# Performance work log

Hardware: AMD Instinct MI355X
Metric: run time of the kernel (lower is better)

Reference implementation:

```python
import jax, jax.numpy as jnp
import numpy as np

B, T, E = 1024, 256, 300  # batch, topic_size, embedding_size


def setup_inputs() -> dict:
    key = jax.random.key(0)
    k1, k2, k3, k4, k5 = jax.random.split(key, 5)
    return {
        "req_theta": jax.random.uniform(k1, (B, T), dtype=jnp.float32),
        "wsdl_theta": jax.random.uniform(k2, (B, T), dtype=jnp.float32),
        "topic_embedding": jax.random.normal(k3, (E, T), dtype=jnp.float32),
        "w_f": jax.random.normal(k4, (T, E), dtype=jnp.float32) * 0.05,
        "b_f": jax.random.normal(k5, (T,), dtype=jnp.float32) * 0.05,
    }


def reference(req_theta, wsdl_theta, topic_embedding, w_f, b_f):
    # topic_embedding: [E, T] -> t(): [T, E]
    t_te = topic_embedding.T  # [T, E]
    # elementwise scale of topic vectors by theta: [B, T, E]
    req_e = req_theta[:, :, None] * t_te
    wsdl_e = wsdl_theta[:, :, None] * t_te
    # f_att: Linear(E, T): [B, T, E] -> [B, T, T]
    req_e = jnp.einsum('bte,fe->btf', req_e, w_f) + b_f
    wsdl_e = jnp.einsum('bte,fe->btf', wsdl_e, w_f) + b_f
    # cross-attention: bmm -> softmax(dim=1) -> permute -> bmm
    att = jnp.einsum('bik,bjk->bij', req_e, wsdl_e)          # [B, T, T]
    att = jax.nn.softmax(att, axis=1)                         # softmax over req dim
    wsdl_att = jnp.einsum('bji,bjk->bik', att, req_e)         # att^T @ req_e
    # mean-pool + cosine similarity * 3
    ave_req = req_e.mean(axis=1)    # [B, T]
    ave_wsdl = wsdl_att.mean(axis=1)  # [B, T]
    eps = 1e-8
    num = jnp.sum(ave_req * ave_wsdl, axis=-1)
    denom = jnp.maximum(jnp.linalg.norm(ave_req, axis=-1) * jnp.linalg.norm(ave_wsdl, axis=-1), eps)
    bi_dist = (num / denom) * 3.0
    return bi_dist
```

## Files before the change

kernel.cpp:

```cpp
#include <hip/hip_runtime.h>
#include <math.h>

constexpr int NB = 1024;
constexpr int NT = 256;
constexpr int NE = 300;

typedef float f32x2 __attribute__((ext_vector_type(2)));
typedef float f32x4 __attribute__((ext_vector_type(4)));

#if defined(__has_builtin)
#if __has_builtin(__builtin_amdgcn_exp2f)
#define EXP2F(x) __builtin_amdgcn_exp2f(x)
#else
#define EXP2F(x) exp2f(x)
#endif
#if __has_builtin(__builtin_amdgcn_logf)
#define LOG2F(x) __builtin_amdgcn_logf(x)
#else
#define LOG2F(x) log2f(x)
#endif
#else
#define EXP2F(x) exp2f(x)
#define LOG2F(x) log2f(x)
#endif

__device__ __forceinline__ float rdlane(float v, int l) {
  return __uint_as_float(__builtin_amdgcn_readlane(__float_as_uint(v), l));
}

__device__ __forceinline__ f32x2 pk_fma_alo(f32x2 a, f32x2 b, f32x2 c) {
  f32x2 d;
  asm("v_pk_fma_f32 %0, %1, %2, %3 op_sel:[0,0,0] op_sel_hi:[0,1,1]"
      : "=v"(d) : "v"(a), "v"(b), "v"(c));
  return d;
}
__device__ __forceinline__ f32x2 pk_fma_ahi(f32x2 a, f32x2 b, f32x2 c) {
  f32x2 d;
  asm("v_pk_fma_f32 %0, %1, %2, %3 op_sel:[1,0,0] op_sel_hi:[1,1,1]"
      : "=v"(d) : "v"(a), "v"(b), "v"(c));
  return d;
}
__device__ __forceinline__ f32x2 pk_fma_chi(f32x2 a, f32x2 b, f32x2 c) {
  f32x2 d;
  asm("v_pk_fma_f32 %0, %1, %2, %3 op_sel:[0,0,1] op_sel_hi:[1,1,1]"
      : "=v"(d) : "v"(a), "v"(b), "v"(c));
  return d;
}

__global__ __launch_bounds__(1024) void k_M(const float* __restrict__ TE,
                                            const float* __restrict__ wf,
                                            float* __restrict__ Mt,
                                            float* __restrict__ Mrow) {
  __shared__ float red[4][NT];
  int tid = threadIdx.x;
  int q = __builtin_amdgcn_readfirstlane(tid >> 8);
  int c = tid & 255, lane = tid & 63, blk = blockIdx.x;

  const float* wrow = wf + blk * NE;
  float4 wa = *(const float4*)(wrow + 4 * lane);
  float4 wb = make_float4(0.f, 0.f, 0.f, 0.f);
  if (lane < 11) wb = *(const float4*)(wrow + 256 + 4 * lane);
  float acc = 0.f;
#pragma unroll
  for (int k = 0; k < 16; ++k) {
    int ec = q + 4 * k;
    float wx = rdlane(wa.x, ec), wy = rdlane(wa.y, ec);
    float wz = rdlane(wa.z, ec), ww = rdlane(wa.w, ec);
    const float* tp = TE + 4 * ec * NT + c;
    acc = fmaf(tp[0], wx, acc);
    acc = fmaf(tp[NT], wy, acc);
    acc = fmaf(tp[2 * NT], wz, acc);
    acc = fmaf(tp[3 * NT], ww, acc);
  }
#pragma unroll
  for (int k = 16; k < 19; ++k) {
    int ec = q + 4 * k;
    if (ec < 75) {
      int l = ec - 64;
      float wx = rdlane(wb.x, l), wy = rdlane(wb.y, l);
      float wz = rdlane(wb.z, l), ww = rdlane(wb.w, l);
      const float* tp = TE + 4 * ec * NT + c;
      acc = fmaf(tp[0], wx, acc);
      acc = fmaf(tp[NT], wy, acc);
      acc = fmaf(tp[2 * NT], wz, acc);
      acc = fmaf(tp[3 * NT], ww, acc);
    }
  }
  red[q][c] = acc;
  __syncthreads();
  if (q == 0) {
    float s = red[0][c] + red[1][c] + red[2][c] + red[3][c];
    Mt[blk * NT + c] = s;
    Mrow[c * NT + blk] = s;
  }
}

__global__ __launch_bounds__(1024) void k_G(const float* __restrict__ Mt,
                                            const float* __restrict__ Mrow,
                                            const float* __restrict__ bf,
                                            float* __restrict__ G2,
                                            float* __restrict__ u2,
                                            float* __restrict__ Gd,
                                            float* __restrict__ Gof) {
  __shared__ float red[4][NT];
  __shared__ float fin2[4][2];
  const float LOG2E = 1.4426950408889634f;
  int tid = threadIdx.x;
  int q = __builtin_amdgcn_readfirstlane(tid >> 8);
  int c = tid & 255, lane = tid & 63, wid = tid >> 6, blk = blockIdx.x;

  const float* mrowp = Mrow + blk * NT;
  float4 ma = *(const float4*)(mrowp + 4 * lane);
  float acc = 0.f;
  int c0 = q * 16;
#pragma unroll
  for (int k = 0; k < 16; ++k) {
    int fc = c0 + k;
    float mx = rdlane(ma.x, fc), my = rdlane(ma.y, fc);
    float mz = rdlane(ma.z, fc), mw = rdlane(ma.w, fc);
    const float* tp = Mt + 4 * fc * NT + c;
    acc = fmaf(tp[0], mx, acc);
    acc = fmaf(tp[NT], my, acc);
    acc = fmaf(tp[2 * NT], mz, acc);
    acc = fmaf(tp[3 * NT], mw, acc);
  }
  red[q][c] = acc;
  __syncthreads();
  if (q == 0) {
    float g = (red[0][c] + red[1][c] + red[2][c] + red[3][c]) * LOG2E;
    G2[blk * NT + c] = g;
    if (c == blk) Gd[blk] = g;
    float v = (c == blk) ? -3.0e38f : g;
#pragma unroll
    for (int off = 32; off > 0; off >>= 1) v = fmaxf(v, __shfl_down(v, off, 64));
    if (lane == 0) fin2[wid][0] = v;
    float p = mrowp[c] * bf[c];
#pragma unroll
    for (int off = 32; off > 0; off >>= 1) p += __shfl_down(p, off, 64);
    if (lane == 0) fin2[wid][1] = p;
  }
  __syncthreads();
  if (tid == 0) {
    float gof = fmaxf(fmaxf(fin2[0][0], fin2[1][0]), fmaxf(fin2[2][0], fin2[3][0]));
    Gof[blk] = fmaxf(gof, 0.f);
    u2[blk] = (fin2[0][1] + fin2[1][1] + fin2[2][1] + fin2[3][1]) * LOG2E;
  }
}

__global__ __launch_bounds__(512, 8) void k_main(
    const float* __restrict__ req, const float* __restrict__ wsdl,
    const float* __restrict__ Mrow, const float* __restrict__ G2,
    const float* __restrict__ u2, const float* __restrict__ Gd,
    const float* __restrict__ Gof, const float* __restrict__ bf,
    float* __restrict__ out) {
  __shared__ f32x2 sArr[NT];
  __shared__ f32x2 WL[NT];
  __shared__ f32x2 QB[NT];
  __shared__ f32x4 MHN4[64];
  __shared__ f32x4 RRB[2][8][64];
  __shared__ float finU[4];
  __shared__ float fin[4][3];

  int tid = threadIdx.x;
  int cq = tid & 63, q = tid >> 6;
  int c4 = cq * 4;
  int b = blockIdx.x, i0 = q * 32;

  if (tid < NT) {
    float r = req[b * NT + tid];
    float u = u2[tid];
    sArr[tid] = (f32x2){r, u};
    WL[tid] = (f32x2){wsdl[b * NT + tid], 0.f};
    float um = fmaxf(u, 0.f);
#pragma unroll
    for (int off = 32; off > 0; off >>= 1) um = fmaxf(um, __shfl_down(um, off, 64));
    if ((tid & 63) == 0) finU[tid >> 6] = um;
  }

  f32x4 rcP = *(const f32x4*)(req + b * NT + c4);
  f32x4 wbP = *(const f32x4*)(wsdl + b * NT + c4);
  f32x4 ucP = *(const f32x4*)(u2 + c4);
  f32x4 gdP = *(const f32x4*)(Gd + c4);
  f32x4 gofP = *(const f32x4*)(Gof + c4);

  __syncthreads();
  float up = fmaxf(fmaxf(finU[0], finU[1]), fmaxf(finU[2], finU[3]));

  f32x4 mhn;
  mhn.x = -fmaxf(rcP.x * fmaf(wbP.x, gdP.x, ucP.x), fmaf(wbP.x, gofP.x, up));
  mhn.y = -fmaxf(rcP.y * fmaf(wbP.y, gdP.y, ucP.y), fmaf(wbP.y, gofP.y, up));
  mhn.z = -fmaxf(rcP.z * fmaf(wbP.z, gdP.z, ucP.z), fmaf(wbP.z, gofP.z, up));
  mhn.w = -fmaxf(rcP.w * fmaf(wbP.w, gdP.w, ucP.w), fmaf(wbP.w, gofP.w, up));
  if (q == 0) MHN4[cq] = mhn;

  f32x2 wb01 = (f32x2){wbP.x, wbP.y}, wb23 = (f32x2){wbP.z, wbP.w};
  f32x2 rc01 = (f32x2){rcP.x, rcP.y}, rc23 = (f32x2){rcP.z, rcP.w};
  f32x2 uc01 = (f32x2){ucP.x, ucP.y}, uc23 = (f32x2){ucP.z, ucP.w};
  f32x2 mhn01 = (f32x2){mhn.x, mhn.y}, mhn23 = (f32x2){mhn.z, mhn.w};

  float d0 = 0.f, d1 = 0.f, d2 = 0.f, d3 = 0.f;
  {
    const float* gp = G2 + i0 * NT + c4;
    const char* sb = (const char*)(sArr + i0);
#pragma unroll 2
    for (int o = 0; o < 8; ++o) {
#pragma unroll
      for (int uu = 0; uu < 4; ++uu) {
        f32x4 gP = *(const f32x4*)(gp + uu * NT);
        f32x2 su = *(const f32x2*)(sb + uu * 8);
        f32x2 g01 = (f32x2){gP.x, gP.y}, g23 = (f32x2){gP.z, gP.w};
        f32x2 t01 = pk_fma_chi(wb01, g01, su);
        f32x2 t23 = pk_fma_chi(wb23, g23, su);
        f32x2 p01 = pk_fma_alo(su, t01, mhn01);
        f32x2 p23 = pk_fma_alo(su, t23, mhn23);
        d0 += EXP2F(p01.x); d1 += EXP2F(p01.y);
        d2 += EXP2F(p23.x); d3 += EXP2F(p23.y);
      }
      gp += 4 * NT;
      sb += 32;
    }
  }
  RRB[0][q][cq] = (f32x4){d0, d1, d2, d3};
  __syncthreads();

  if (tid < NT) {
    const float* rb = (const float*)RRB;
    float den = rb[tid];
#pragma unroll
    for (int k = 1; k < 8; ++k) den += rb[k * 256 + tid];
    float nl = ((const float*)MHN4)[tid] - LOG2F(den);
    ((float*)(WL + tid))[1] = nl;
  }
  __syncthreads();

  float S0 = 0.f, S1 = 0.f, S2 = 0.f, S3 = 0.f;
  {
    const float* gp = G2 + i0 * NT + c4;
    const char* wb_ = (const char*)(WL + i0);
#pragma unroll 2
    for (int o = 0; o < 8; ++o) {
#pragma unroll
      for (int uu = 0; uu < 4; ++uu) {
        f32x4 gP = *(const f32x4*)(gp + uu * NT);
        f32x2 wl = *(const f32x2*)(wb_ + uu * 8);
        f32x2 g01 = (f32x2){gP.x, gP.y}, g23 = (f32x2){gP.z, gP.w};
        f32x2 t01 = pk_fma_alo(wl, g01, uc01);
        f32x2 t23 = pk_fma_alo(wl, g23, uc23);
        f32x2 p01 = pk_fma_chi(rc01, t01, wl);
        f32x2 p23 = pk_fma_chi(rc23, t23, wl);
        S0 += EXP2F(p01.x); S1 += EXP2F(p01.y);
        S2 += EXP2F(p23.x); S3 += EXP2F(p23.y);
      }
      gp += 4 * NT;
      wb_ += 32;
    }
  }
  RRB[0][q][cq] = (f32x4){S0, S1, S2, S3};
  __syncthreads();

  if (tid < NT) {
    const float* rb = (const float*)RRB;
    float Sr = rb[tid];
#pragma unroll
    for (int k = 1; k < 8; ++k) Sr += rb[k * 256 + tid];
    f32x2 ru = sArr[tid];
    QB[tid] = (f32x2){ru.x, ru.x * Sr};
  }
  __syncthreads();

  f32x2 a01 = (f32x2){0.f, 0.f}, a23 = a01, y01 = a01, y23 = a01;
  {
    const float* mp = Mrow + i0 * NT + c4;
    const char* qb_ = (const char*)(QB + i0);
#pragma unroll 2
    for (int o = 0; o < 8; ++o) {
#pragma unroll
      for (int uu = 0; uu < 4; ++uu) {
        f32x4 mkP = *(const f32x4*)(mp + uu * NT);
        f32x2 qb = *(const f32x2*)(qb_ + uu * 8);
        f32x2 mk01 = (f32x2){mkP.x, mkP.y}, mk23 = (f32x2){mkP.z, mkP.w};
        a01 = pk_fma_alo(qb, mk01, a01);
        a23 = pk_fma_alo(qb, mk23, a23);
        y01 = pk_fma_ahi(qb, mk01, y01);
        y23 = pk_fma_ahi(qb, mk23, y23);
      }
      mp += 4 * NT;
      qb_ += 32;
    }
  }
  RRB[0][q][cq] = (f32x4){a01.x, a01.y, a23.x, a23.y};
  RRB[1][q][cq] = (f32x4){y01.x, y01.y, y23.x, y23.y};
  __syncthreads();

  if (tid < NT) {
    const float* rb = (const float*)RRB;
    float A = rb[tid], Y = rb[2048 + tid];
#pragma unroll
    for (int k = 1; k < 8; ++k) {
      A += rb[k * 256 + tid];
      Y += rb[2048 + k * 256 + tid];
    }
    float bfc = bf[tid];
    const float invT = 1.0f / NT;
    float avr = fmaf(A, invT, bfc);
    float avw = fmaf(Y, invT, bfc);
    float sn = avr * avw, sa = avr * avr, sc = avw * avw;
#pragma unroll
    for (int off = 32; off > 0; off >>= 1) {
      sn += __shfl_down(sn, off, 64);
      sa += __shfl_down(sa, off, 64);
      sc += __shfl_down(sc, off, 64);
    }
    if ((tid & 63) == 0) {
      int w = tid >> 6;
      fin[w][0] = sn;
      fin[w][1] = sa;
      fin[w][2] = sc;
    }
  }
  __syncthreads();
  if (tid == 0) {
    float N = fin[0][0] + fin[1][0] + fin[2][0] + fin[3][0];
    float A = fin[0][1] + fin[1][1] + fin[2][1] + fin[3][1];
    float C = fin[0][2] + fin[1][2] + fin[2][2] + fin[3][2];
    out[b] = N / fmaxf(sqrtf(A) * sqrtf(C), 1e-8f) * 3.0f;
  }
}

extern "C" void kernel_launch(void* const* d_in, const int* in_sizes, int n_in,
                              void* d_out, int out_size, void* d_ws, size_t ws_size,
                              hipStream_t stream) {
  const float* req  = (const float*)d_in[0];
  const float* wsdl = (const float*)d_in[1];
  const float* TE   = (const float*)d_in[2];
  const float* wf   = (const float*)d_in[3];
  const float* bf   = (const float*)d_in[4];
  float* out = (float*)d_out;

  float* Mt   = (float*)d_ws;
  float* Mrow = Mt + NT * NT;
  float* G2   = Mrow + NT * NT;
  float* u2   = G2 + NT * NT;
  float* Gd   = u2 + NT;
  float* Gof  = Gd + NT;

  k_M<<<NT, 1024, 0, stream>>>(TE, wf, Mt, Mrow);
  k_G<<<NT, 1024, 0, stream>>>(Mt, Mrow, bf, G2, u2, Gd, Gof);
  k_main<<<NB, 512, 0, stream>>>(req, wsdl, Mrow, G2, u2, Gd, Gof, bf, out);
}
```

Baseline: 102.7 us.

## Process two batch rows per block to reuse G2 and Mrow loads

Each k_main block now handles two batch elements, so every G2 and Mrow tile loaded from global memory feeds computation for both rows. Shared-memory buffers widen to f32x4 to hold per-batch values, and the grid shrinks to 512 blocks. This halves global/L2 traffic for the shared matrices, at the cost of higher register use (launch bounds relaxed from 8 to 4) and fewer blocks to fill the GPU.

```diff
diff --git a/kernel.cpp b/kernel.cpp
--- a/kernel.cpp
+++ b/kernel.cpp
@@ -4,6 +4,7 @@
 constexpr int NB = 1024;
 constexpr int NT = 256;
 constexpr int NE = 300;
+constexpr int NBATCH = 2;
 
 typedef float f32x2 __attribute__((ext_vector_type(2)));
 typedef float f32x4 __attribute__((ext_vector_type(4)));
@@ -28,6 +29,11 @@
   return __uint_as_float(__builtin_amdgcn_readlane(__float_as_uint(v), l));
 }
 
+__device__ __forceinline__ f32x2 pk_fma(f32x2 a, f32x2 b, f32x2 c) {
+  f32x2 d;
+  asm("v_pk_fma_f32 %0, %1, %2, %3" : "=v"(d) : "v"(a), "v"(b), "v"(c));
+  return d;
+}
 __device__ __forceinline__ f32x2 pk_fma_alo(f32x2 a, f32x2 b, f32x2 c) {
   f32x2 d;
   asm("v_pk_fma_f32 %0, %1, %2, %3 op_sel:[0,0,0] op_sel_hi:[0,1,1]"
@@ -37,6 +43,12 @@
 __device__ __forceinline__ f32x2 pk_fma_ahi(f32x2 a, f32x2 b, f32x2 c) {
   f32x2 d;
   asm("v_pk_fma_f32 %0, %1, %2, %3 op_sel:[1,0,0] op_sel_hi:[1,1,1]"
+      : "=v"(d) : "v"(a), "v"(b), "v"(c));
+  return d;
+}
+__device__ __forceinline__ f32x2 pk_fma_clo(f32x2 a, f32x2 b, f32x2 c) {
+  f32x2 d;
+  asm("v_pk_fma_f32 %0, %1, %2, %3 op_sel:[0,0,0] op_sel_hi:[1,1,0]"
       : "=v"(d) : "v"(a), "v"(b), "v"(c));
   return d;
 }
@@ -147,38 +159,40 @@
   }
 }
 
-__global__ __launch_bounds__(512, 8) void k_main(
+__global__ __launch_bounds__(512, 4) void k_main(
     const float* __restrict__ req, const float* __restrict__ wsdl,
     const float* __restrict__ Mrow, const float* __restrict__ G2,
     const float* __restrict__ u2, const float* __restrict__ Gd,
     const float* __restrict__ Gof, const float* __restrict__ bf,
     float* __restrict__ out) {
-  __shared__ f32x2 sArr[NT];
-  __shared__ f32x2 WL[NT];
-  __shared__ f32x2 QB[NT];
-  __shared__ f32x4 MHN4[64];
-  __shared__ f32x4 RRB[2][8][64];
+  __shared__ f32x4 sArr[NT];
+  __shared__ f32x4 WL[NT];
+  __shared__ f32x4 QB[NT];
+  __shared__ f32x4 MHN[2][64];
+  __shared__ f32x4 RRB[4][8][64];
   __shared__ float finU[4];
-  __shared__ float fin[4][3];
+  __shared__ float fin[4][6];
 
   int tid = threadIdx.x;
   int cq = tid & 63, q = tid >> 6;
   int c4 = cq * 4;
-  int b = blockIdx.x, i0 = q * 32;
+  int blk = blockIdx.x, b0 = blk * NBATCH, i0 = q * 32;
 
   if (tid < NT) {
-    float r = req[b * NT + tid];
+    float r0 = req[b0 * NT + tid], r1 = req[(b0 + 1) * NT + tid];
     float u = u2[tid];
-    sArr[tid] = (f32x2){r, u};
-    WL[tid] = (f32x2){wsdl[b * NT + tid], 0.f};
+    sArr[tid] = (f32x4){r0, r1, u, u};
+    WL[tid] = (f32x4){wsdl[b0 * NT + tid], wsdl[(b0 + 1) * NT + tid], 0.f, 0.f};
     float um = fmaxf(u, 0.f);
 #pragma unroll
     for (int off = 32; off > 0; off >>= 1) um = fmaxf(um, __shfl_down(um, off, 64));
     if ((tid & 63) == 0) finU[tid >> 6] = um;
   }
 
-  f32x4 rcP = *(const f32x4*)(req + b * NT + c4);
-  f32x4 wbP = *(const f32x4*)(wsdl + b * NT + c4);
+  f32x4 rc0P = *(const f32x4*)(req + b0 * NT + c4);
+  f32x4 rc1P = *(const f32x4*)(req + (b0 + 1) * NT + c4);
+  f32x4 wb0P = *(const f32x4*)(wsdl + b0 * NT + c4);
+  f32x4 wb1P = *(const f32x4*)(wsdl + (b0 + 1) * NT + c4);
   f32x4 ucP = *(const f32x4*)(u2 + c4);
   f32x4 gdP = *(const f32x4*)(Gd + c4);
   f32x4 gofP = *(const f32x4*)(Gof + c4);
@@ -186,19 +200,30 @@
   __syncthreads();
   float up = fmaxf(fmaxf(finU[0], finU[1]), fmaxf(finU[2], finU[3]));
 
-  f32x4 mhn;
-  mhn.x = -fmaxf(rcP.x * fmaf(wbP.x, gdP.x, ucP.x), fmaf(wbP.x, gofP.x, up));
-  mhn.y = -fmaxf(rcP.y * fmaf(wbP.y, gdP.y, ucP.y), fmaf(wbP.y, gofP.y, up));
-  mhn.z = -fmaxf(rcP.z * fmaf(wbP.z, gdP.z, ucP.z), fmaf(wbP.z, gofP.z, up));
-  mhn.w = -fmaxf(rcP.w * fmaf(wbP.w, gdP.w, ucP.w), fmaf(wbP.w, gofP.w, up));
-  if (q == 0) MHN4[cq] = mhn;
-
-  f32x2 wb01 = (f32x2){wbP.x, wbP.y}, wb23 = (f32x2){wbP.z, wbP.w};
-  f32x2 rc01 = (f32x2){rcP.x, rcP.y}, rc23 = (f32x2){rcP.z, rcP.w};
+  f32x4 mhn0, mhn1;
+  mhn0.x = -fmaxf(rc0P.x * fmaf(wb0P.x, gdP.x, ucP.x), fmaf(wb0P.x, gofP.x, up));
+  mhn0.y = -fmaxf(rc0P.y * fmaf(wb0P.y, gdP.y, ucP.y), fmaf(wb0P.y, gofP.y, up));
+  mhn0.z = -fmaxf(rc0P.z * fmaf(wb0P.z, gdP.z, ucP.z), fmaf(wb0P.z, gofP.z, up));
+  mhn0.w = -fmaxf(rc0P.w * fmaf(wb0P.w, gdP.w, ucP.w), fmaf(wb0P.w, gofP.w, up));
+  mhn1.x = -fmaxf(rc1P.x * fmaf(wb1P.x, gdP.x, ucP.x), fmaf(wb1P.x, gofP.x, up));
+  mhn1.y = -fmaxf(rc1P.y * fmaf(wb1P.y, gdP.y, ucP.y), fmaf(wb1P.y, gofP.y, up));
+  mhn1.z = -fmaxf(rc1P.z * fmaf(wb1P.z, gdP.z, ucP.z), fmaf(wb1P.z, gofP.z, up));
+  mhn1.w = -fmaxf(rc1P.w * fmaf(wb1P.w, gdP.w, ucP.w), fmaf(wb1P.w, gofP.w, up));
+  if (q == 0) {
+    MHN[0][cq] = mhn0;
+    MHN[1][cq] = mhn1;
+  }
+
+  f32x2 wb0_01 = (f32x2){wb0P.x, wb0P.y}, wb0_23 = (f32x2){wb0P.z, wb0P.w};
+  f32x2 wb1_01 = (f32x2){wb1P.x, wb1P.y}, wb1_23 = (f32x2){wb1P.z, wb1P.w};
+  f32x2 rc0_01 = (f32x2){rc0P.x, rc0P.y}, rc0_23 = (f32x2){rc0P.z, rc0P.w};
+  f32x2 rc1_01 = (f32x2){rc1P.x, rc1P.y}, rc1_23 = (f32x2){rc1P.z, rc1P.w};
   f32x2 uc01 = (f32x2){ucP.x, ucP.y}, uc23 = (f32x2){ucP.z, ucP.w};
-  f32x2 mhn01 = (f32x2){mhn.x, mhn.y}, mhn23 = (f32x2){mhn.z, mhn.w};
-
-  float d0 = 0.f, d1 = 0.f, d2 = 0.f, d3 = 0.f;
+  f32x2 mhn0_01 = (f32x2){mhn0.x, mhn0.y}, mhn0_23 = (f32x2){mhn0.z, mhn0.w};
+  f32x2 mhn1_01 = (f32x2){mhn1.x, mhn1.y}, mhn1_23 = (f32x2){mhn1.z, mhn1.w};
+
+  float d00 = 0.f, d01 = 0.f, d02 = 0.f, d03 = 0.f;
+  float d10 = 0.f, d11 = 0.f, d12 = 0.f, d13 = 0.f;
   {
     const float* gp = G2 + i0 * NT + c4;
     const char* sb = (const char*)(sArr + i0);
@@ -207,33 +232,48 @@
 #pragma unroll
       for (int uu = 0; uu < 4; ++uu) {
         f32x4 gP = *(const f32x4*)(gp + uu * NT);
-        f32x2 su = *(const f32x2*)(sb + uu * 8);
+        f32x4 su = *(const f32x4*)(sb + uu * 16);
+        f32x2 su_lo = (f32x2){su.x, su.y};
+        f32x2 uu_ = (f32x2){su.z, su.w};
         f32x2 g01 = (f32x2){gP.x, gP.y}, g23 = (f32x2){gP.z, gP.w};
-        f32x2 t01 = pk_fma_chi(wb01, g01, su);
-        f32x2 t23 = pk_fma_chi(wb23, g23, su);
-        f32x2 p01 = pk_fma_alo(su, t01, mhn01);
-        f32x2 p23 = pk_fma_alo(su, t23, mhn23);
-        d0 += EXP2F(p01.x); d1 += EXP2F(p01.y);
-        d2 += EXP2F(p23.x); d3 += EXP2F(p23.y);
+        f32x2 t0_01 = pk_fma(wb0_01, g01, uu_);
+        f32x2 t0_23 = pk_fma(wb0_23, g23, uu_);
+        f32x2 t1_01 = pk_fma(wb1_01, g01, uu_);
+        f32x2 t1_23 = pk_fma(wb1_23, g23, uu_);
+        f32x2 p0_01 = pk_fma_alo(su_lo, t0_01, mhn0_01);
+        f32x2 p0_23 = pk_fma_alo(su_lo, t0_23, mhn0_23);
+        f32x2 p1_01 = pk_fma_ahi(su_lo, t1_01, mhn1_01);
+        f32x2 p1_23 = pk_fma_ahi(su_lo, t1_23, mhn1_23);
+        d00 += EXP2F(p0_01.x); d01 += EXP2F(p0_01.y);
+        d02 += EXP2F(p0_23.x); d03 += EXP2F(p0_23.y);
+        d10 += EXP2F(p1_01.x); d11 += EXP2F(p1_01.y);
+        d12 += EXP2F(p1_23.x); d13 += EXP2F(p1_23.y);
       }
       gp += 4 * NT;
-      sb += 32;
-    }
-  }
-  RRB[0][q][cq] = (f32x4){d0, d1, d2, d3};
+      sb += 64;
+    }
+  }
+  RRB[0][q][cq] = (f32x4){d00, d01, d02, d03};
+  RRB[1][q][cq] = (f32x4){d10, d11, d12, d13};
   __syncthreads();
 
   if (tid < NT) {
     const float* rb = (const float*)RRB;
-    float den = rb[tid];
-#pragma unroll
-    for (int k = 1; k < 8; ++k) den += rb[k * 256 + tid];
-    float nl = ((const float*)MHN4)[tid] - LOG2F(den);
-    ((float*)(WL + tid))[1] = nl;
-  }
-  __syncthreads();
-
-  float S0 = 0.f, S1 = 0.f, S2 = 0.f, S3 = 0.f;
+    float den0 = rb[tid], den1 = rb[2048 + tid];
+#pragma unroll
+    for (int k = 1; k < 8; ++k) {
+      den0 += rb[k * 256 + tid];
+      den1 += rb[2048 + k * 256 + tid];
+    }
+    float nl0 = ((const float*)MHN)[tid] - LOG2F(den0);
+    float nl1 = ((const float*)MHN)[256 + tid] - LOG2F(den1);
+    ((float*)(WL + tid))[2] = nl0;
+    ((float*)(WL + tid))[3] = nl1;
+  }
+  __syncthreads();
+
+  float S00 = 0.f, S01 = 0.f, S02 = 0.f, S03 = 0.f;
+  float S10 = 0.f, S11 = 0.f, S12 = 0.f, S13 = 0.f;
   {
     const float* gp = G2 + i0 * NT + c4;
     const char* wb_ = (const char*)(WL + i0);
@@ -242,33 +282,46 @@
 #pragma unroll
       for (int uu = 0; uu < 4; ++uu) {
         f32x4 gP = *(const f32x4*)(gp + uu * NT);
-        f32x2 wl = *(const f32x2*)(wb_ + uu * 8);
+        f32x4 wl = *(const f32x4*)(wb_ + uu * 16);
+        f32x2 wl_lo = (f32x2){wl.x, wl.y};
+        f32x2 wl_hi = (f32x2){wl.z, wl.w};
         f32x2 g01 = (f32x2){gP.x, gP.y}, g23 = (f32x2){gP.z, gP.w};
-        f32x2 t01 = pk_fma_alo(wl, g01, uc01);
-        f32x2 t23 = pk_fma_alo(wl, g23, uc23);
-        f32x2 p01 = pk_fma_chi(rc01, t01, wl);
-        f32x2 p23 = pk_fma_chi(rc23, t23, wl);
-        S0 += EXP2F(p01.x); S1 += EXP2F(p01.y);
-        S2 += EXP2F(p23.x); S3 += EXP2F(p23.y);
+        f32x2 t0_01 = pk_fma_alo(wl_lo, g01, uc01);
+        f32x2 t0_23 = pk_fma_alo(wl_lo, g23, uc23);
+        f32x2 t1_01 = pk_fma_ahi(wl_lo, g01, uc01);
+        f32x2 t1_23 = pk_fma_ahi(wl_lo, g23, uc23);
+        f32x2 p0_01 = pk_fma_clo(rc0_01, t0_01, wl_hi);
+        f32x2 p0_23 = pk_fma_clo(rc0_23, t0_23, wl_hi);
+        f32x2 p1_01 = pk_fma_chi(rc1_01, t1_01, wl_hi);
+        f32x2 p1_23 = pk_fma_chi(rc1_23, t1_23, wl_hi);
+        S00 += EXP2F(p0_01.x); S01 += EXP2F(p0_01.y);
+        S02 += EXP2F(p0_23.x); S03 += EXP2F(p0_23.y);
+        S10 += EXP2F(p1_01.x); S11 += EXP2F(p1_01.y);
+        S12 += EXP2F(p1_23.x); S13 += EXP2F(p1_23.y);
       }
       gp += 4 * NT;
-      wb_ += 32;
-    }
-  }
-  RRB[0][q][cq] = (f32x4){S0, S1, S2, S3};
+      wb_ += 64;
+    }
+  }
+  RRB[0][q][cq] = (f32x4){S00, S01, S02, S03};
+  RRB[1][q][cq] = (f32x4){S10, S11, S12, S13};
   __syncthreads();
 
   if (tid < NT) {
     const float* rb = (const float*)RRB;
-    float Sr = rb[tid];
-#pragma unroll
-    for (int k = 1; k < 8; ++k) Sr += rb[k * 256 + tid];
-    f32x2 ru = sArr[tid];
-    QB[tid] = (f32x2){ru.x, ru.x * Sr};
-  }
-  __syncthreads();
-
-  f32x2 a01 = (f32x2){0.f, 0.f}, a23 = a01, y01 = a01, y23 = a01;
+    float Sr0 = rb[tid], Sr1 = rb[2048 + tid];
+#pragma unroll
+    for (int k = 1; k < 8; ++k) {
+      Sr0 += rb[k * 256 + tid];
+      Sr1 += rb[2048 + k * 256 + tid];
+    }
+    f32x4 ru = sArr[tid];
+    QB[tid] = (f32x4){ru.x, ru.y, ru.x * Sr0, ru.y * Sr1};
+  }
+  __syncthreads();
+
+  f32x2 a0_01 = (f32x2){0.f, 0.f}, a0_23 = a0_01, a1_01 = a0_01, a1_23 = a0_01;
+  f32x2 y0_01 = a0_01, y0_23 = a0_01, y1_01 = a0_01, y1_23 = a0_01;
   {
     const float* mp = Mrow + i0 * NT + c4;
     const char* qb_ = (const char*)(QB + i0);
@@ -277,53 +330,70 @@
 #pragma unroll
       for (int uu = 0; uu < 4; ++uu) {
         f32x4 mkP = *(const f32x4*)(mp + uu * NT);
-        f32x2 qb = *(const f32x2*)(qb_ + uu * 8);
+        f32x4 qb = *(const f32x4*)(qb_ + uu * 16);
+        f32x2 qb_lo = (f32x2){qb.x, qb.y};
+        f32x2 qb_hi = (f32x2){qb.z, qb.w};
         f32x2 mk01 = (f32x2){mkP.x, mkP.y}, mk23 = (f32x2){mkP.z, mkP.w};
-        a01 = pk_fma_alo(qb, mk01, a01);
-        a23 = pk_fma_alo(qb, mk23, a23);
-        y01 = pk_fma_ahi(qb, mk01, y01);
-        y23 = pk_fma_ahi(qb, mk23, y23);
+        a0_01 = pk_fma_alo(qb_lo, mk01, a0_01);
+        a0_23 = pk_fma_alo(qb_lo, mk23, a0_23);
+        a1_01 = pk_fma_ahi(qb_lo, mk01, a1_01);
+        a1_23 = pk_fma_ahi(qb_lo, mk23, a1_23);
+        y0_01 = pk_fma_alo(qb_hi, mk01, y0_01);
+        y0_23 = pk_fma_alo(qb_hi, mk23, y0_23);
+        y1_01 = pk_fma_ahi(qb_hi, mk01, y1_01);
+        y1_23 = pk_fma_ahi(qb_hi, mk23, y1_23);
       }
       mp += 4 * NT;
-      qb_ += 32;
-    }
-  }
-  RRB[0][q][cq] = (f32x4){a01.x, a01.y, a23.x, a23.y};
-  RRB[1][q][cq] = (f32x4){y01.x, y01.y, y23.x, y23.y};
+      qb_ += 64;
+    }
+  }
+  RRB[0][q][cq] = (f32x4){a0_01.x, a0_01.y, a0_23.x, a0_23.y};
+  RRB[1][q][cq] = (f32x4){a1_01.x, a1_01.y, a1_23.x, a1_23.y};
+  RRB[2][q][cq] = (f32x4){y0_01.x, y0_01.y, y0_23.x, y0_23.y};
+  RRB[3][q][cq] = (f32x4){y1_01.x, y1_01.y, y1_23.x, y1_23.y};
   __syncthreads();
 
   if (tid < NT) {
     const float* rb = (const float*)RRB;
-    float A = rb[tid], Y = rb[2048 + tid];
+    float A0 = rb[tid], A1 = rb[2048 + tid];
+    float Y0 = rb[4096 + tid], Y1 = rb[6144 + tid];
 #pragma unroll
     for (int k = 1; k < 8; ++k) {
-      A += rb[k * 256 + tid];
-      Y += rb[2048 + k * 256 + tid];
+      A0 += rb[k * 256 + tid];
+      A1 += rb[2048 + k * 256 + tid];
+      Y0 += rb[4096 + k * 256 + tid];
+      Y1 += rb[6144 + k * 256 + tid];
     }
     float bfc = bf[tid];
     const float invT = 1.0f / NT;
-    float avr = fmaf(A, invT, bfc);
-    float avw = fmaf(Y, invT, bfc);
-    float sn = avr * avw, sa = avr * avr, sc = avw * avw;
-#pragma unroll
-    for (int off = 32; off > 0; off >>= 1) {
-      sn += __shfl_down(sn, off, 64);
-      sa += __shfl_down(sa, off, 64);
-      sc += __shfl_down(sc, off, 64);
-    }
+    float avr0 = fmaf(A0, invT, bfc);
+    float avr1 = fmaf(A1, invT, bfc);
+    float avw0 = fmaf(Y0, invT, bfc);
+    float avw1 = fmaf(Y1, invT, bfc);
+    float st[6];
+    st[0] = avr0 * avw0; st[1] = avr0 * avr0; st[2] = avw0 * avw0;
+    st[3] = avr1 * avw1; st[4] = avr1 * avr1; st[5] = avw1 * avw1;
+#pragma unroll
+    for (int k = 0; k < 6; ++k)
+#pragma unroll
+      for (int off = 32; off > 0; off >>= 1) st[k] += __shfl_down(st[k], off, 64);
     if ((tid & 63) == 0) {
       int w = tid >> 6;
-      fin[w][0] = sn;
-      fin[w][1] = sa;
-      fin[w][2] = sc;
-    }
-  }
-  __syncthreads();
-  if (tid == 0) {
-    float N = fin[0][0] + fin[1][0] + fin[2][0] + fin[3][0];
-    float A = fin[0][1] + fin[1][1] + fin[2][1] + fin[3][1];
-    float C = fin[0][2] + fin[1][2] + fin[2][2] + fin[3][2];
-    out[b] = N / fmaxf(sqrtf(A) * sqrtf(C), 1e-8f) * 3.0f;
+#pragma unroll
+      for (int k = 0; k < 6; ++k) fin[w][k] = st[k];
+    }
+  }
+  __syncthreads();
+  if (tid < NBATCH) {
+    int bb = tid;
+    float N = 0.f, A = 0.f, C = 0.f;
+#pragma unroll
+    for (int w = 0; w < 4; ++w) {
+      N += fin[w][3 * bb + 0];
+      A += fin[w][3 * bb + 1];
+      C += fin[w][3 * bb + 2];
+    }
+    out[b0 + bb] = N / fmaxf(sqrtf(A) * sqrtf(C), 1e-8f) * 3.0f;
   }
 }
 
@@ -346,5 +416,6 @@
 
   k_M<<<NT, 1024, 0, stream>>>(TE, wf, Mt, Mrow);
   k_G<<<NT, 1024, 0, stream>>>(Mt, Mrow, bf, G2, u2, Gd, Gof);
-  k_main<<<NB, 512, 0, stream>>>(req, wsdl, Mrow, G2, u2, Gd, Gof, bf, out);
-}
+  k_main<<<NB / NBATCH, 512, 0, stream>>>(req, wsdl, Mrow, G2, u2, Gd, Gof,
+                                          bf, out);
+}
```

New measurement: 94.87 us. -7.6%, faster.

## Process four batch rows per block to reuse G2 and Mrow loads

Applied to the files above, without the earlier changes.

Each k_main block now handles four batch elements instead of one. Every G2/Mrow tile read from global memory or cache is reused across four batches through packed FMAs, and the per-batch vectors are interleaved in shared memory. This cuts the repeated 256x256 matrix streaming per batch. In exchange the grid shrinks to 256 blocks, which is about one per CU, register pressure rises (launch bounds relaxed to 2), and more barriers are added in the epilogue.

```diff
diff --git a/kernel.cpp b/kernel.cpp
--- a/kernel.cpp
+++ b/kernel.cpp
@@ -4,6 +4,7 @@
 constexpr int NB = 1024;
 constexpr int NT = 256;
 constexpr int NE = 300;
+constexpr int NBATCH = 4;
 
 typedef float f32x2 __attribute__((ext_vector_type(2)));
 typedef float f32x4 __attribute__((ext_vector_type(4)));
@@ -28,6 +29,11 @@
   return __uint_as_float(__builtin_amdgcn_readlane(__float_as_uint(v), l));
 }
 
+__device__ __forceinline__ f32x2 pk_fma(f32x2 a, f32x2 b, f32x2 c) {
+  f32x2 d;
+  asm("v_pk_fma_f32 %0, %1, %2, %3" : "=v"(d) : "v"(a), "v"(b), "v"(c));
+  return d;
+}
 __device__ __forceinline__ f32x2 pk_fma_alo(f32x2 a, f32x2 b, f32x2 c) {
   f32x2 d;
   asm("v_pk_fma_f32 %0, %1, %2, %3 op_sel:[0,0,0] op_sel_hi:[0,1,1]"
@@ -37,6 +43,12 @@
 __device__ __forceinline__ f32x2 pk_fma_ahi(f32x2 a, f32x2 b, f32x2 c) {
   f32x2 d;
   asm("v_pk_fma_f32 %0, %1, %2, %3 op_sel:[1,0,0] op_sel_hi:[1,1,1]"
+      : "=v"(d) : "v"(a), "v"(b), "v"(c));
+  return d;
+}
+__device__ __forceinline__ f32x2 pk_fma_clo(f32x2 a, f32x2 b, f32x2 c) {
+  f32x2 d;
+  asm("v_pk_fma_f32 %0, %1, %2, %3 op_sel:[0,0,0] op_sel_hi:[1,1,0]"
       : "=v"(d) : "v"(a), "v"(b), "v"(c));
   return d;
 }
@@ -147,38 +159,50 @@
   }
 }
 
-__global__ __launch_bounds__(512, 8) void k_main(
+__global__ __launch_bounds__(512, 2) void k_main(
     const float* __restrict__ req, const float* __restrict__ wsdl,
     const float* __restrict__ Mrow, const float* __restrict__ G2,
     const float* __restrict__ u2, const float* __restrict__ Gd,
     const float* __restrict__ Gof, const float* __restrict__ bf,
     float* __restrict__ out) {
-  __shared__ f32x2 sArr[NT];
-  __shared__ f32x2 WL[NT];
-  __shared__ f32x2 QB[NT];
-  __shared__ f32x4 MHN4[64];
-  __shared__ f32x4 RRB[2][8][64];
+  __shared__ f32x4 Rs[NT];
+  __shared__ f32x2 Us[NT];
+  __shared__ f32x4 Ws[NT];
+  __shared__ f32x4 NLs[NT];
+  __shared__ f32x4 QBq[NT];
+  __shared__ f32x4 MHN[4][64];
+  __shared__ f32x4 RRB[4][8][64];
+  __shared__ float Avr[4 * NT];
   __shared__ float finU[4];
-  __shared__ float fin[4][3];
+  __shared__ float fin[8][3];
+  float* Avw = (float*)MHN;
 
   int tid = threadIdx.x;
   int cq = tid & 63, q = tid >> 6;
   int c4 = cq * 4;
-  int b = blockIdx.x, i0 = q * 32;
+  int blk = blockIdx.x, b0 = blk * NBATCH, i0 = q * 32;
+  int bsel = tid >> 8, col = tid & 255;
 
   if (tid < NT) {
-    float r = req[b * NT + tid];
+    float r0 = req[(b0 + 0) * NT + tid], r1 = req[(b0 + 1) * NT + tid];
+    float r2 = req[(b0 + 2) * NT + tid], r3 = req[(b0 + 3) * NT + tid];
     float u = u2[tid];
-    sArr[tid] = (f32x2){r, u};
-    WL[tid] = (f32x2){wsdl[b * NT + tid], 0.f};
+    Rs[tid] = (f32x4){r0, r1, r2, r3};
+    Us[tid] = (f32x2){u, u};
+    Ws[tid] = (f32x4){wsdl[(b0 + 0) * NT + tid], wsdl[(b0 + 1) * NT + tid],
+                      wsdl[(b0 + 2) * NT + tid], wsdl[(b0 + 3) * NT + tid]};
     float um = fmaxf(u, 0.f);
 #pragma unroll
     for (int off = 32; off > 0; off >>= 1) um = fmaxf(um, __shfl_down(um, off, 64));
     if ((tid & 63) == 0) finU[tid >> 6] = um;
   }
 
-  f32x4 rcP = *(const f32x4*)(req + b * NT + c4);
-  f32x4 wbP = *(const f32x4*)(wsdl + b * NT + c4);
+  f32x4 rcQ[NBATCH], wbQ[NBATCH];
+#pragma unroll
+  for (int b = 0; b < NBATCH; ++b) {
+    rcQ[b] = *(const f32x4*)(req + (b0 + b) * NT + c4);
+    wbQ[b] = *(const f32x4*)(wsdl + (b0 + b) * NT + c4);
+  }
   f32x4 ucP = *(const f32x4*)(u2 + c4);
   f32x4 gdP = *(const f32x4*)(Gd + c4);
   f32x4 gofP = *(const f32x4*)(Gof + c4);
@@ -186,124 +210,204 @@
   __syncthreads();
   float up = fmaxf(fmaxf(finU[0], finU[1]), fmaxf(finU[2], finU[3]));
 
-  f32x4 mhn;
-  mhn.x = -fmaxf(rcP.x * fmaf(wbP.x, gdP.x, ucP.x), fmaf(wbP.x, gofP.x, up));
-  mhn.y = -fmaxf(rcP.y * fmaf(wbP.y, gdP.y, ucP.y), fmaf(wbP.y, gofP.y, up));
-  mhn.z = -fmaxf(rcP.z * fmaf(wbP.z, gdP.z, ucP.z), fmaf(wbP.z, gofP.z, up));
-  mhn.w = -fmaxf(rcP.w * fmaf(wbP.w, gdP.w, ucP.w), fmaf(wbP.w, gofP.w, up));
-  if (q == 0) MHN4[cq] = mhn;
-
-  f32x2 wb01 = (f32x2){wbP.x, wbP.y}, wb23 = (f32x2){wbP.z, wbP.w};
-  f32x2 rc01 = (f32x2){rcP.x, rcP.y}, rc23 = (f32x2){rcP.z, rcP.w};
+  f32x2 wb01[NBATCH], wb23[NBATCH], rc01[NBATCH], rc23[NBATCH];
+  f32x2 mh01[NBATCH], mh23[NBATCH];
+#pragma unroll
+  for (int b = 0; b < NBATCH; ++b) {
+    f32x4 mhn;
+    mhn.x = -fmaxf(rcQ[b].x * fmaf(wbQ[b].x, gdP.x, ucP.x), fmaf(wbQ[b].x, gofP.x, up));
+    mhn.y = -fmaxf(rcQ[b].y * fmaf(wbQ[b].y, gdP.y, ucP.y), fmaf(wbQ[b].y, gofP.y, up));
+    mhn.z = -fmaxf(rcQ[b].z * fmaf(wbQ[b].z, gdP.z, ucP.z), fmaf(wbQ[b].z, gofP.z, up));
+    mhn.w = -fmaxf(rcQ[b].w * fmaf(wbQ[b].w, gdP.w, ucP.w), fmaf(wbQ[b].w, gofP.w, up));
+    if (q == 0) MHN[b][cq] = mhn;
+    mh01[b] = (f32x2){mhn.x, mhn.y};
+    mh23[b] = (f32x2){mhn.z, mhn.w};
+    wb01[b] = (f32x2){wbQ[b].x, wbQ[b].y};
+    wb23[b] = (f32x2){wbQ[b].z, wbQ[b].w};
+    rc01[b] = (f32x2){rcQ[b].x, rcQ[b].y};
+    rc23[b] = (f32x2){rcQ[b].z, rcQ[b].w};
+  }
   f32x2 uc01 = (f32x2){ucP.x, ucP.y}, uc23 = (f32x2){ucP.z, ucP.w};
-  f32x2 mhn01 = (f32x2){mhn.x, mhn.y}, mhn23 = (f32x2){mhn.z, mhn.w};
-
-  float d0 = 0.f, d1 = 0.f, d2 = 0.f, d3 = 0.f;
+
+  f32x2 dA[NBATCH], dB[NBATCH];
+#pragma unroll
+  for (int b = 0; b < NBATCH; ++b) dA[b] = dB[b] = (f32x2){0.f, 0.f};
   {
     const float* gp = G2 + i0 * NT + c4;
-    const char* sb = (const char*)(sArr + i0);
+    const char* rb_ = (const char*)(Rs + i0);
+    const char* ub_ = (const char*)(Us + i0);
 #pragma unroll 2
     for (int o = 0; o < 8; ++o) {
 #pragma unroll
       for (int uu = 0; uu < 4; ++uu) {
         f32x4 gP = *(const f32x4*)(gp + uu * NT);
-        f32x2 su = *(const f32x2*)(sb + uu * 8);
+        f32x4 ru = *(const f32x4*)(rb_ + uu * 16);
+        f32x2 uP = *(const f32x2*)(ub_ + uu * 8);
         f32x2 g01 = (f32x2){gP.x, gP.y}, g23 = (f32x2){gP.z, gP.w};
-        f32x2 t01 = pk_fma_chi(wb01, g01, su);
-        f32x2 t23 = pk_fma_chi(wb23, g23, su);
-        f32x2 p01 = pk_fma_alo(su, t01, mhn01);
-        f32x2 p23 = pk_fma_alo(su, t23, mhn23);
-        d0 += EXP2F(p01.x); d1 += EXP2F(p01.y);
-        d2 += EXP2F(p23.x); d3 += EXP2F(p23.y);
+        f32x2 r01 = (f32x2){ru.x, ru.y}, r23 = (f32x2){ru.z, ru.w};
+#pragma unroll
+        for (int b = 0; b < NBATCH; ++b) {
+          f32x2 rp = (b < 2) ? r01 : r23;
+          f32x2 t01 = pk_fma(wb01[b], g01, uP);
+          f32x2 t23 = pk_fma(wb23[b], g23, uP);
+          f32x2 p01 = (b & 1) ? pk_fma_ahi(rp, t01, mh01[b])
+                              : pk_fma_alo(rp, t01, mh01[b]);
+          f32x2 p23 = (b & 1) ? pk_fma_ahi(rp, t23, mh23[b])
+                              : pk_fma_alo(rp, t23, mh23[b]);
+          dA[b] += (f32x2){EXP2F(p01.x), EXP2F(p01.y)};
+          dB[b] += (f32x2){EXP2F(p23.x), EXP2F(p23.y)};
+        }
       }
       gp += 4 * NT;
-      sb += 32;
-    }
-  }
-  RRB[0][q][cq] = (f32x4){d0, d1, d2, d3};
-  __syncthreads();
-
-  if (tid < NT) {
-    const float* rb = (const float*)RRB;
-    float den = rb[tid];
-#pragma unroll
-    for (int k = 1; k < 8; ++k) den += rb[k * 256 + tid];
-    float nl = ((const float*)MHN4)[tid] - LOG2F(den);
-    ((float*)(WL + tid))[1] = nl;
-  }
-  __syncthreads();
-
-  float S0 = 0.f, S1 = 0.f, S2 = 0.f, S3 = 0.f;
+      rb_ += 64;
+      ub_ += 32;
+    }
+  }
+#pragma unroll
+  for (int b = 0; b < NBATCH; ++b)
+    RRB[b][q][cq] = (f32x4){dA[b].x, dA[b].y, dB[b].x, dB[b].y};
+  __syncthreads();
+
+#pragma unroll
+  for (int k2 = 0; k2 < 2; ++k2) {
+    int b = 2 * k2 + bsel;
+    const float* rb = (const float*)RRB + b * 2048;
+    float den = rb[col];
+#pragma unroll
+    for (int k = 1; k < 8; ++k) den += rb[k * 256 + col];
+    float nl = ((const float*)MHN)[b * 256 + col] - LOG2F(den);
+    ((float*)(NLs + col))[b] = nl;
+  }
+  __syncthreads();
+
+  f32x2 SA[NBATCH], SB[NBATCH];
+#pragma unroll
+  for (int b = 0; b < NBATCH; ++b) SA[b] = SB[b] = (f32x2){0.f, 0.f};
   {
     const float* gp = G2 + i0 * NT + c4;
-    const char* wb_ = (const char*)(WL + i0);
+    const char* wb_ = (const char*)(Ws + i0);
+    const char* nb_ = (const char*)(NLs + i0);
 #pragma unroll 2
     for (int o = 0; o < 8; ++o) {
 #pragma unroll
       for (int uu = 0; uu < 4; ++uu) {
         f32x4 gP = *(const f32x4*)(gp + uu * NT);
-        f32x2 wl = *(const f32x2*)(wb_ + uu * 8);
+        f32x4 wq = *(const f32x4*)(wb_ + uu * 16);
+        f32x4 nq = *(const f32x4*)(nb_ + uu * 16);
         f32x2 g01 = (f32x2){gP.x, gP.y}, g23 = (f32x2){gP.z, gP.w};
-        f32x2 t01 = pk_fma_alo(wl, g01, uc01);
-        f32x2 t23 = pk_fma_alo(wl, g23, uc23);
-        f32x2 p01 = pk_fma_chi(rc01, t01, wl);
-        f32x2 p23 = pk_fma_chi(rc23, t23, wl);
-        S0 += EXP2F(p01.x); S1 += EXP2F(p01.y);
-        S2 += EXP2F(p23.x); S3 += EXP2F(p23.y);
+        f32x2 w01 = (f32x2){wq.x, wq.y}, w23 = (f32x2){wq.z, wq.w};
+        f32x2 n01 = (f32x2){nq.x, nq.y}, n23 = (f32x2){nq.z, nq.w};
+#pragma unroll
+        for (int b = 0; b < NBATCH; ++b) {
+          f32x2 wp = (b < 2) ? w01 : w23;
+          f32x2 np = (b < 2) ? n01 : n23;
+          f32x2 t01 = (b & 1) ? pk_fma_ahi(wp, g01, uc01)
+                              : pk_fma_alo(wp, g01, uc01);
+          f32x2 t23 = (b & 1) ? pk_fma_ahi(wp, g23, uc23)
+                              : pk_fma_alo(wp, g23, uc23);
+          f32x2 p01 = (b & 1) ? pk_fma_chi(rc01[b], t01, np)
+                              : pk_fma_clo(rc01[b], t01, np);
+          f32x2 p23 = (b & 1) ? pk_fma_chi(rc23[b], t23, np)
+                              : pk_fma_clo(rc23[b], t23, np);
+          SA[b] += (f32x2){EXP2F(p01.x), EXP2F(p01.y)};
+          SB[b] += (f32x2){EXP2F(p23.x), EXP2F(p23.y)};
+        }
       }
       gp += 4 * NT;
-      wb_ += 32;
-    }
-  }
-  RRB[0][q][cq] = (f32x4){S0, S1, S2, S3};
-  __syncthreads();
-
-  if (tid < NT) {
-    const float* rb = (const float*)RRB;
-    float Sr = rb[tid];
-#pragma unroll
-    for (int k = 1; k < 8; ++k) Sr += rb[k * 256 + tid];
-    f32x2 ru = sArr[tid];
-    QB[tid] = (f32x2){ru.x, ru.x * Sr};
-  }
-  __syncthreads();
-
-  f32x2 a01 = (f32x2){0.f, 0.f}, a23 = a01, y01 = a01, y23 = a01;
+      wb_ += 64;
+      nb_ += 64;
+    }
+  }
+#pragma unroll
+  for (int b = 0; b < NBATCH; ++b)
+    RRB[b][q][cq] = (f32x4){SA[b].x, SA[b].y, SB[b].x, SB[b].y};
+  __syncthreads();
+
+#pragma unroll
+  for (int k2 = 0; k2 < 2; ++k2) {
+    int b = 2 * k2 + bsel;
+    const float* rb = (const float*)RRB + b * 2048;
+    float Sr = rb[col];
+#pragma unroll
+    for (int k = 1; k < 8; ++k) Sr += rb[k * 256 + col];
+    float r = ((const float*)(Rs + col))[b];
+    ((float*)(QBq + col))[b] = r * Sr;
+  }
+  __syncthreads();
+
+  f32x2 aA[NBATCH], aB[NBATCH], yA[NBATCH], yB[NBATCH];
+#pragma unroll
+  for (int b = 0; b < NBATCH; ++b)
+    aA[b] = aB[b] = yA[b] = yB[b] = (f32x2){0.f, 0.f};
   {
     const float* mp = Mrow + i0 * NT + c4;
-    const char* qb_ = (const char*)(QB + i0);
+    const char* rb_ = (const char*)(Rs + i0);
+    const char* qb_ = (const char*)(QBq + i0);
 #pragma unroll 2
     for (int o = 0; o < 8; ++o) {
 #pragma unroll
       for (int uu = 0; uu < 4; ++uu) {
         f32x4 mkP = *(const f32x4*)(mp + uu * NT);
-        f32x2 qb = *(const f32x2*)(qb_ + uu * 8);
+        f32x4 rq = *(const f32x4*)(rb_ + uu * 16);
+        f32x4 qq = *(const f32x4*)(qb_ + uu * 16);
         f32x2 mk01 = (f32x2){mkP.x, mkP.y}, mk23 = (f32x2){mkP.z, mkP.w};
-        a01 = pk_fma_alo(qb, mk01, a01);
-        a23 = pk_fma_alo(qb, mk23, a23);
-        y01 = pk_fma_ahi(qb, mk01, y01);
-        y23 = pk_fma_ahi(qb, mk23, y23);
+        f32x2 r01 = (f32x2){rq.x, rq.y}, r23 = (f32x2){rq.z, rq.w};
+        f32x2 q01 = (f32x2){qq.x, qq.y}, q23 = (f32x2){qq.z, qq.w};
+#pragma unroll
+        for (int b = 0; b < NBATCH; ++b) {
+          f32x2 rp = (b < 2) ? r01 : r23;
+          f32x2 qp = (b < 2) ? q01 : q23;
+          aA[b] = (b & 1) ? pk_fma_ahi(rp, mk01, aA[b])
+                          : pk_fma_alo(rp, mk01, aA[b]);
+          aB[b] = (b & 1) ? pk_fma_ahi(rp, mk23, aB[b])
+                          : pk_fma_alo(rp, mk23, aB[b]);
+          yA[b] = (b & 1) ? pk_fma_ahi(qp, mk01, yA[b])
+                          : pk_fma_alo(qp, mk01, yA[b]);
+          yB[b] = (b & 1) ? pk_fma_ahi(qp, mk23, yB[b])
+                          : pk_fma_alo(qp, mk23, yB[b]);
+        }
       }
       mp += 4 * NT;
-      qb_ += 32;
-    }
-  }
-  RRB[0][q][cq] = (f32x4){a01.x, a01.y, a23.x, a23.y};
-  RRB[1][q][cq] = (f32x4){y01.x, y01.y, y23.x, y23.y};
-  __syncthreads();
-
-  if (tid < NT) {
-    const float* rb = (const float*)RRB;
-    float A = rb[tid], Y = rb[2048 + tid];
-#pragma unroll
-    for (int k = 1; k < 8; ++k) {
-      A += rb[k * 256 + tid];
-      Y += rb[2048 + k * 256 + tid];
-    }
-    float bfc = bf[tid];
-    const float invT = 1.0f / NT;
-    float avr = fmaf(A, invT, bfc);
-    float avw = fmaf(Y, invT, bfc);
+      rb_ += 64;
+      qb_ += 64;
+    }
+  }
+  const float invT = 1.0f / NT;
+  float bfc = bf[col];
+#pragma unroll
+  for (int b = 0; b < NBATCH; ++b)
+    RRB[b][q][cq] = (f32x4){aA[b].x, aA[b].y, aB[b].x, aB[b].y};
+  __syncthreads();
+#pragma unroll
+  for (int k2 = 0; k2 < 2; ++k2) {
+    int b = 2 * k2 + bsel;
+    const float* rb = (const float*)RRB + b * 2048;
+    float A = rb[col];
+#pragma unroll
+    for (int k = 1; k < 8; ++k) A += rb[k * 256 + col];
+    Avr[b * 256 + col] = fmaf(A, invT, bfc);
+  }
+  __syncthreads();
+#pragma unroll
+  for (int b = 0; b < NBATCH; ++b)
+    RRB[b][q][cq] = (f32x4){yA[b].x, yA[b].y, yB[b].x, yB[b].y};
+  __syncthreads();
+#pragma unroll
+  for (int k2 = 0; k2 < 2; ++k2) {
+    int b = 2 * k2 + bsel;
+    const float* rb = (const float*)RRB + b * 2048;
+    float Y = rb[col];
+#pragma unroll
+    for (int k = 1; k < 8; ++k) Y += rb[k * 256 + col];
+    Avw[b * 256 + col] = fmaf(Y, invT, bfc);
+  }
+  __syncthreads();
+
+#pragma unroll
+  for (int p = 0; p < 2; ++p) {
+    int b = 2 * p + bsel;
+    float avr = Avr[b * 256 + col];
+    float avw = Avw[b * 256 + col];
     float sn = avr * avw, sa = avr * avr, sc = avw * avw;
 #pragma unroll
     for (int off = 32; off > 0; off >>= 1) {
@@ -317,13 +421,18 @@
       fin[w][1] = sa;
       fin[w][2] = sc;
     }
-  }
-  __syncthreads();
-  if (tid == 0) {
-    float N = fin[0][0] + fin[1][0] + fin[2][0] + fin[3][0];
-    float A = fin[0][1] + fin[1][1] + fin[2][1] + fin[3][1];
-    float C = fin[0][2] + fin[1][2] + fin[2][2] + fin[3][2];
-    out[b] = N / fmaxf(sqrtf(A) * sqrtf(C), 1e-8f) * 3.0f;
+    __syncthreads();
+    if (tid < 2) {
+      float N = 0.f, A = 0.f, C = 0.f;
+#pragma unroll
+      for (int w = 0; w < 4; ++w) {
+        N += fin[tid * 4 + w][0];
+        A += fin[tid * 4 + w][1];
+        C += fin[tid * 4 + w][2];
+      }
+      out[b0 + 2 * p + tid] = N / fmaxf(sqrtf(A) * sqrtf(C), 1e-8f) * 3.0f;
+    }
+    __syncthreads();
   }
 }
 
@@ -346,5 +455,6 @@
 
   k_M<<<NT, 1024, 0, stream>>>(TE, wf, Mt, Mrow);
   k_G<<<NT, 1024, 0, stream>>>(Mt, Mrow, bf, G2, u2, Gd, Gof);
-  k_main<<<NB, 512, 0, stream>>>(req, wsdl, Mrow, G2, u2, Gd, Gof, bf, out);
-}
+  k_main<<<NB / NBATCH, 512, 0, stream>>>(req, wsdl, Mrow, G2, u2, Gd, Gof,
+                                          bf, out);
+}
```

Result: slower. 106.5 us (+3.7%).
